# Kernel optimization log

Hardware: AMD Instinct MI355X
Metric: run time of the kernel (lower is better)

Reference implementation:

```python
import jax, jax.numpy as jnp
import numpy as np

ROT = 256  # Hadamard block size (ConvLinear4bit._n)


def _hadamard(n):
    # Sylvester construction of the n x n Hadamard matrix (n power of 2)
    H = np.array([[1.0]], dtype=np.float32)
    while H.shape[0] < n:
        H = np.block([[H, H], [H, -H]])
    return jnp.asarray(H / np.sqrt(n), dtype=jnp.float32)


def setup_inputs() -> dict:
    key = jax.random.key(0)
    k1, k2, k3, k4 = jax.random.split(key, 4)
    N, D_in, D_out = 4096, 4096, 4096
    x = jax.random.normal(k1, (N, D_in), dtype=jnp.float32)
    # unpacked int4 weights in [-7, 7] (logical content of the packed uint8 buffer)
    weight_int = jax.random.randint(k2, (D_out, D_in), -7, 8, dtype=jnp.int32)
    # per-output-row weight scales (quarot: max|W_rot| / 7)
    w_scale = jax.random.uniform(k3, (D_out, 1), dtype=jnp.float32) * 0.01 + 1e-4
    bias = jax.random.normal(k4, (D_out,), dtype=jnp.float32) * 0.01
    return {"x": x, "weight_int": weight_int, "w_scale": w_scale, "bias": bias}


def reference(x, weight_int, w_scale, bias):
    N, D = x.shape
    H = _hadamard(ROT)
    # blockwise Hadamard rotation along the feature dim (D is a multiple of ROT)
    x_rot = (x.reshape(N, D // ROT, ROT) @ H).reshape(N, D)
    # per-row symmetric int4 quantization of activations
    scales_x = jnp.max(jnp.abs(x_rot), axis=-1, keepdims=True) / 7.0  # [N, 1]
    q_x = jnp.clip(jnp.round(x_rot / scales_x), -8, 7).astype(jnp.int32)
    acc = jnp.matmul(q_x, weight_int.T)
    # sym_dequant: row scale (activations) * col scale (weights), then bias
    out = acc.astype(jnp.float32) * scales_x * w_scale.T + bias
    return out
```

## Files before the change

### kernel.cpp

```cpp
#include <hip/hip_runtime.h>
#include <math.h>

typedef int v4i  __attribute__((ext_vector_type(4)));
typedef int v16i __attribute__((ext_vector_type(16)));

#define DIM 4096
#define BM 256
#define BK 128
#define ATILE (BM * BK)
#define BUFSZ (2 * ATILE)

__device__ __forceinline__ void async16(const void* g, void* l) {
    __builtin_amdgcn_global_load_lds((__attribute__((address_space(1))) void*)(g),
                                     (__attribute__((address_space(3))) void*)(l),
                                     16, 0, 0);
}

#define VMCNT(N) asm volatile("s_waitcnt vmcnt(" #N ")" ::: "memory")
#define BARRIER() asm volatile("s_barrier" ::: "memory")

__global__ __launch_bounds__(256) void prep(const float* __restrict__ x,
                                            const int* __restrict__ w,
                                            signed char* __restrict__ q,
                                            signed char* __restrict__ w8,
                                            float* __restrict__ scales) {
    if (blockIdx.x >= 4096) {
        int i = (blockIdx.x - 4096) * 256 + threadIdx.x;
        int4 v = ((const int4*)w)[i];
        char4 c;
        c.x = (signed char)v.x; c.y = (signed char)v.y;
        c.z = (signed char)v.z; c.w = (signed char)v.w;
        ((char4*)w8)[i] = c;
        return;
    }
    const int row  = blockIdx.x;
    const int lane = threadIdx.x & 63;
    const int wave = threadIdx.x >> 6;
    const float4* xr4 = (const float4*)(x + (size_t)row * DIM);

    float sgn[6];
    #pragma unroll
    for (int i = 0; i < 6; ++i) sgn[i] = (lane & (1 << i)) ? -1.0f : 1.0f;

    float f[4][4];
    #pragma unroll
    for (int b = 0; b < 4; ++b) {
        const int blk = wave + 4 * b;
        float4 v = xr4[blk * 64 + lane];
        float t0 = v.x + v.y, t1 = v.x - v.y;
        float t2 = v.z + v.w, t3 = v.z - v.w;
        f[b][0] = t0 + t2; f[b][1] = t1 + t3;
        f[b][2] = t0 - t2; f[b][3] = t1 - t3;
        #pragma unroll
        for (int st = 0; st < 6; ++st) {
            const int m = 1 << st;
            #pragma unroll
            for (int j = 0; j < 4; ++j) {
                float p = __shfl_xor(f[b][j], m, 64);
                f[b][j] = fmaf(sgn[st], f[b][j], p);
            }
        }
    }

    float m = 0.0f;
    #pragma unroll
    for (int b = 0; b < 4; ++b)
        #pragma unroll
        for (int j = 0; j < 4; ++j) m = fmaxf(m, fabsf(f[b][j]));
    #pragma unroll
    for (int d = 32; d; d >>= 1) m = fmaxf(m, __shfl_xor(m, d, 64));
    __shared__ float sm[4];
    if (lane == 0) sm[wave] = m;
    __syncthreads();
    m = fmaxf(fmaxf(sm[0], sm[1]), fmaxf(sm[2], sm[3]));

    const float s = (m * 0.0625f) / 7.0f;
    if (threadIdx.x == 0) scales[row] = s;
    const float rinv = 7.0f / m;

    char4* qr4 = (char4*)(q + (size_t)row * DIM);
    #pragma unroll
    for (int b = 0; b < 4; ++b) {
        const int blk = wave + 4 * b;
        char4 c;
        int qi;
        qi = (int)rintf(f[b][0] * rinv); c.x = (signed char)min(7, max(-8, qi));
        qi = (int)rintf(f[b][1] * rinv); c.y = (signed char)min(7, max(-8, qi));
        qi = (int)rintf(f[b][2] * rinv); c.z = (signed char)min(7, max(-8, qi));
        qi = (int)rintf(f[b][3] * rinv); c.w = (signed char)min(7, max(-8, qi));
        qr4[blk * 64 + lane] = c;
    }
}

__global__ __launch_bounds__(512, 2) void gemm_q8(const signed char* __restrict__ A,
                                                  const signed char* __restrict__ B,
                                                  const float* __restrict__ rowScale,
                                                  const float* __restrict__ wscale,
                                                  const float* __restrict__ bias,
                                                  float* __restrict__ out) {
    __shared__ __align__(16) signed char S[2 * BUFSZ];

    const int flat = blockIdx.y * gridDim.x + blockIdx.x;
    const int xcd  = flat & 7;
    const int idx  = flat >> 3;
    const int bm   = ((xcd >> 1) << 2) + (idx & 3);
    const int bn   = ((xcd & 1) << 3) + (idx >> 2);

    const int t = threadIdx.x;
    const int lane = t & 63;
    const int wave = t >> 6;
    const int wm = (wave >> 2) * 128;
    const int wn = (wave & 3) * 64;
    const int l31 = lane & 31, lh = lane >> 5;

    const signed char* ga[4];
    const signed char* gb[4];
    int ldsA[4], ldsB[4];
    #pragma unroll
    for (int h = 0; h < 4; ++h) {
        const int cidx = t + 512 * h;
        const int row  = cidx >> 3;
        const int g    = (cidx & 7) ^ (row & 7);
        ga[h] = A + (size_t)(bm * BM + row) * DIM + g * 16;
        gb[h] = B + (size_t)(bn * BM + row) * DIM + g * 16;
        ldsA[h] = cidx * 16;
        ldsB[h] = ATILE + cidx * 16;
    }

    int offA[4][4], offB[2][4];
    #pragma unroll
    for (int i = 0; i < 4; ++i)
        #pragma unroll
        for (int s = 0; s < 4; ++s) {
            const int r = wm + i * 32 + l31;
            offA[i][s] = r * BK + (((2 * s + lh) ^ (r & 7)) * 16);
        }
    #pragma unroll
    for (int j = 0; j < 2; ++j)
        #pragma unroll
        for (int s = 0; s < 4; ++s) {
            const int c = wn + j * 32 + l31;
            offB[j][s] = ATILE + c * BK + (((2 * s + lh) ^ (c & 7)) * 16);
        }

    v16i acc[4][2] = {};

#define STAGE(P) do {                                                          \
        _Pragma("unroll")                                                      \
        for (int h = 0; h < 4; ++h) {                                          \
            async16(ga[h], &S[(P) * BUFSZ + ldsA[h]]); ga[h] += BK;            \
            async16(gb[h], &S[(P) * BUFSZ + ldsB[h]]); gb[h] += BK;            \
        }                                                                      \
    } while (0)

#define COMPUTE(P) do {                                                        \
        __builtin_amdgcn_s_setprio(1);                                         \
        _Pragma("unroll")                                                      \
        for (int s = 0; s < 4; ++s) {                                          \
            const v4i a0 = *(const v4i*)&S[(P) * BUFSZ + offA[0][s]];          \
            const v4i a1 = *(const v4i*)&S[(P) * BUFSZ + offA[1][s]];          \
            const v4i a2 = *(const v4i*)&S[(P) * BUFSZ + offA[2][s]];          \
            const v4i a3 = *(const v4i*)&S[(P) * BUFSZ + offA[3][s]];          \
            const v4i b0 = *(const v4i*)&S[(P) * BUFSZ + offB[0][s]];          \
            const v4i b1 = *(const v4i*)&S[(P) * BUFSZ + offB[1][s]];          \
            acc[0][0] = __builtin_amdgcn_mfma_i32_32x32x32_i8(a0, b0, acc[0][0], 0, 0, 0); \
            acc[0][1] = __builtin_amdgcn_mfma_i32_32x32x32_i8(a0, b1, acc[0][1], 0, 0, 0); \
            acc[1][0] = __builtin_amdgcn_mfma_i32_32x32x32_i8(a1, b0, acc[1][0], 0, 0, 0); \
            acc[1][1] = __builtin_amdgcn_mfma_i32_32x32x32_i8(a1, b1, acc[1][1], 0, 0, 0); \
            acc[2][0] = __builtin_amdgcn_mfma_i32_32x32x32_i8(a2, b0, acc[2][0], 0, 0, 0); \
            acc[2][1] = __builtin_amdgcn_mfma_i32_32x32x32_i8(a2, b1, acc[2][1], 0, 0, 0); \
            acc[3][0] = __builtin_amdgcn_mfma_i32_32x32x32_i8(a3, b0, acc[3][0], 0, 0, 0); \
            acc[3][1] = __builtin_amdgcn_mfma_i32_32x32x32_i8(a3, b1, acc[3][1], 0, 0, 0); \
        }                                                                      \
        __builtin_amdgcn_s_setprio(0);                                         \
    } while (0)

    STAGE(0);
    #pragma unroll 1
    for (int it = 0; it < 15; ++it) {
        STAGE(1); VMCNT(8); BARRIER(); COMPUTE(0); BARRIER();
        STAGE(0); VMCNT(8); BARRIER(); COMPUTE(1); BARRIER();
    }
    STAGE(1); VMCNT(8); BARRIER(); COMPUTE(0); BARRIER();
    VMCNT(0); BARRIER(); COMPUTE(1);

#undef STAGE
#undef COMPUTE

    #pragma unroll
    for (int j = 0; j < 2; ++j) {
        const int col = bn * BM + wn + j * 32 + l31;
        const float ws = wscale[col];
        const float bs = bias[col];
        #pragma unroll
        for (int i = 0; i < 4; ++i) {
            const int rb = bm * BM + wm + i * 32 + 4 * lh;
            #pragma unroll
            for (int r = 0; r < 16; ++r) {
                const int row = rb + (r & 3) + 8 * (r >> 2);
                out[(size_t)row * DIM + col] =
                    ((float)acc[i][j][r] * rowScale[row]) * ws + bs;
            }
        }
    }
}

extern "C" void kernel_launch(void* const* d_in, const int* in_sizes, int n_in,
                              void* d_out, int out_size, void* d_ws, size_t ws_size,
                              hipStream_t stream) {
    const float* x      = (const float*)d_in[0];
    const int*   wint   = (const int*)d_in[1];
    const float* wscale = (const float*)d_in[2];
    const float* bias   = (const float*)d_in[3];
    float* out = (float*)d_out;

    signed char* q8 = (signed char*)d_ws;
    signed char* w8 = q8 + (size_t)DIM * DIM;
    float* sx = (float*)(w8 + (size_t)DIM * DIM);

    prep<<<4096 + 16384, 256, 0, stream>>>(x, wint, q8, w8, sx);
    gemm_q8<<<dim3(DIM / BM, DIM / BM), 512, 0, stream>>>(q8, w8, sx, wscale, bias, out);
}
```

Measured before the change: 266.3 us.

## Load B fragments directly to registers and triple-buffer A in LDS with BK=64

The GEMM no longer stages the weight tile through LDS. Each wave loads its B fragments straight from global memory into registers, rotating through three register sets. A tiles are kept in LDS in a fragment-native layout, using three rotating buffers of K=64 with one barrier per stage, replacing the previous double-buffered K=128 swizzled layout. The goal is to cut LDS traffic, LDS footprint and the number of barriers. The cost is extra VGPRs and uncoalesced global reads of B that depend on L2 hits, with no LDS sharing of B across the two waves that use the same columns.

New measurement: 284.1 us. +6.7%, slower.

```diff
diff --git a/kernel.cpp b/kernel.cpp
--- a/kernel.cpp
+++ b/kernel.cpp
@@ -6,9 +6,8 @@
 
 #define DIM 4096
 #define BM 256
-#define BK 128
-#define ATILE (BM * BK)
-#define BUFSZ (2 * ATILE)
+#define BK 64
+#define ABUF 16384
 
 __device__ __forceinline__ void async16(const void* g, void* l) {
     __builtin_amdgcn_global_load_lds((__attribute__((address_space(1))) void*)(g),
@@ -98,7 +97,7 @@
                                                   const float* __restrict__ wscale,
                                                   const float* __restrict__ bias,
                                                   float* __restrict__ out) {
-    __shared__ __align__(16) signed char S[2 * BUFSZ];
+    __shared__ __align__(16) signed char S[3 * ABUF];
 
     const int flat = blockIdx.y * gridDim.x + blockIdx.x;
     const int xcd  = flat & 7;
@@ -113,78 +112,109 @@
     const int wn = (wave & 3) * 64;
     const int l31 = lane & 31, lh = lane >> 5;
 
-    const signed char* ga[4];
-    const signed char* gb[4];
-    int ldsA[4], ldsB[4];
-    #pragma unroll
-    for (int h = 0; h < 4; ++h) {
+    const signed char* ga[2];
+    int ldsA[2];
+    #pragma unroll
+    for (int h = 0; h < 2; ++h) {
         const int cidx = t + 512 * h;
-        const int row  = cidx >> 3;
-        const int g    = (cidx & 7) ^ (row & 7);
-        ga[h] = A + (size_t)(bm * BM + row) * DIM + g * 16;
-        gb[h] = B + (size_t)(bn * BM + row) * DIM + g * 16;
+        const int b    = cidx >> 6;
+        const int g    = b >> 1;
+        const int sH   = b & 1;
+        const int l    = cidx & 63;
+        const int row  = g * 32 + (l & 31);
+        const int kb   = sH * 32 + (l >> 5) * 16;
+        ga[h] = A + (size_t)(bm * BM + row) * DIM + kb;
         ldsA[h] = cidx * 16;
-        ldsB[h] = ATILE + cidx * 16;
-    }
-
-    int offA[4][4], offB[2][4];
-    #pragma unroll
-    for (int i = 0; i < 4; ++i)
-        #pragma unroll
-        for (int s = 0; s < 4; ++s) {
-            const int r = wm + i * 32 + l31;
-            offA[i][s] = r * BK + (((2 * s + lh) ^ (r & 7)) * 16);
-        }
+    }
+
+    const signed char* pb[4];
     #pragma unroll
     for (int j = 0; j < 2; ++j)
         #pragma unroll
-        for (int s = 0; s < 4; ++s) {
-            const int c = wn + j * 32 + l31;
-            offB[j][s] = ATILE + c * BK + (((2 * s + lh) ^ (c & 7)) * 16);
-        }
+        for (int s = 0; s < 2; ++s)
+            pb[j * 2 + s] = B + (size_t)(bn * BM + wn + j * 32 + l31) * DIM
+                              + s * 32 + lh * 16;
+
+    const signed char* rbA = &S[(wave >> 2) * 8192 + lane * 16];
 
     v16i acc[4][2] = {};
-
-#define STAGE(P) do {                                                          \
-        _Pragma("unroll")                                                      \
-        for (int h = 0; h < 4; ++h) {                                          \
-            async16(ga[h], &S[(P) * BUFSZ + ldsA[h]]); ga[h] += BK;            \
-            async16(gb[h], &S[(P) * BUFSZ + ldsB[h]]); gb[h] += BK;            \
+    v4i b0[4], b1[4], b2[4];
+
+#define STAGE_A(P3) do {                                                       \
+        async16(ga[0], &S[(P3) * ABUF + ldsA[0]]); ga[0] += BK;                \
+        async16(ga[1], &S[(P3) * ABUF + ldsA[1]]); ga[1] += BK;                \
+    } while (0)
+
+#define B_LOAD(BS) do {                                                        \
+        BS[0] = *(const v4i*)pb[0]; pb[0] += BK;                               \
+        BS[1] = *(const v4i*)pb[1]; pb[1] += BK;                               \
+        BS[2] = *(const v4i*)pb[2]; pb[2] += BK;                               \
+        BS[3] = *(const v4i*)pb[3]; pb[3] += BK;                               \
+    } while (0)
+
+#define COMPUTE(P3, BS) do {                                                   \
+        const signed char* rb = rbA + (P3) * ABUF;                             \
+        __builtin_amdgcn_s_setprio(1);                                         \
+        {                                                                      \
+            const v4i a0 = *(const v4i*)(rb);                                  \
+            const v4i a1 = *(const v4i*)(rb + 2048);                           \
+            const v4i a2 = *(const v4i*)(rb + 4096);                           \
+            const v4i a3 = *(const v4i*)(rb + 6144);                           \
+            acc[0][0] = __builtin_amdgcn_mfma_i32_32x32x32_i8(a0, BS[0], acc[0][0], 0, 0, 0); \
+            acc[0][1] = __builtin_amdgcn_mfma_i32_32x32x32_i8(a0, BS[2], acc[0][1], 0, 0, 0); \
+            acc[1][0] = __builtin_amdgcn_mfma_i32_32x32x32_i8(a1, BS[0], acc[1][0], 0, 0, 0); \
+            acc[1][1] = __builtin_amdgcn_mfma_i32_32x32x32_i8(a1, BS[2], acc[1][1], 0, 0, 0); \
+            acc[2][0] = __builtin_amdgcn_mfma_i32_32x32x32_i8(a2, BS[0], acc[2][0], 0, 0, 0); \
+            acc[2][1] = __builtin_amdgcn_mfma_i32_32x32x32_i8(a2, BS[2], acc[2][1], 0, 0, 0); \
+            acc[3][0] = __builtin_amdgcn_mfma_i32_32x32x32_i8(a3, BS[0], acc[3][0], 0, 0, 0); \
+            acc[3][1] = __builtin_amdgcn_mfma_i32_32x32x32_i8(a3, BS[2], acc[3][1], 0, 0, 0); \
         }                                                                      \
-    } while (0)
-
-#define COMPUTE(P) do {                                                        \
-        __builtin_amdgcn_s_setprio(1);                                         \
-        _Pragma("unroll")                                                      \
-        for (int s = 0; s < 4; ++s) {                                          \
-            const v4i a0 = *(const v4i*)&S[(P) * BUFSZ + offA[0][s]];          \
-            const v4i a1 = *(const v4i*)&S[(P) * BUFSZ + offA[1][s]];          \
-            const v4i a2 = *(const v4i*)&S[(P) * BUFSZ + offA[2][s]];          \
-            const v4i a3 = *(const v4i*)&S[(P) * BUFSZ + offA[3][s]];          \
-            const v4i b0 = *(const v4i*)&S[(P) * BUFSZ + offB[0][s]];          \
-            const v4i b1 = *(const v4i*)&S[(P) * BUFSZ + offB[1][s]];          \
-            acc[0][0] = __builtin_amdgcn_mfma_i32_32x32x32_i8(a0, b0, acc[0][0], 0, 0, 0); \
-            acc[0][1] = __builtin_amdgcn_mfma_i32_32x32x32_i8(a0, b1, acc[0][1], 0, 0, 0); \
-            acc[1][0] = __builtin_amdgcn_mfma_i32_32x32x32_i8(a1, b0, acc[1][0], 0, 0, 0); \
-            acc[1][1] = __builtin_amdgcn_mfma_i32_32x32x32_i8(a1, b1, acc[1][1], 0, 0, 0); \
-            acc[2][0] = __builtin_amdgcn_mfma_i32_32x32x32_i8(a2, b0, acc[2][0], 0, 0, 0); \
-            acc[2][1] = __builtin_amdgcn_mfma_i32_32x32x32_i8(a2, b1, acc[2][1], 0, 0, 0); \
-            acc[3][0] = __builtin_amdgcn_mfma_i32_32x32x32_i8(a3, b0, acc[3][0], 0, 0, 0); \
-            acc[3][1] = __builtin_amdgcn_mfma_i32_32x32x32_i8(a3, b1, acc[3][1], 0, 0, 0); \
+        {                                                                      \
+            const v4i a0 = *(const v4i*)(rb + 1024);                           \
+            const v4i a1 = *(const v4i*)(rb + 3072);                           \
+            const v4i a2 = *(const v4i*)(rb + 5120);                           \
+            const v4i a3 = *(const v4i*)(rb + 7168);                           \
+            acc[0][0] = __builtin_amdgcn_mfma_i32_32x32x32_i8(a0, BS[1], acc[0][0], 0, 0, 0); \
+            acc[0][1] = __builtin_amdgcn_mfma_i32_32x32x32_i8(a0, BS[3], acc[0][1], 0, 0, 0); \
+            acc[1][0] = __builtin_amdgcn_mfma_i32_32x32x32_i8(a1, BS[1], acc[1][0], 0, 0, 0); \
+            acc[1][1] = __builtin_amdgcn_mfma_i32_32x32x32_i8(a1, BS[3], acc[1][1], 0, 0, 0); \
+            acc[2][0] = __builtin_amdgcn_mfma_i32_32x32x32_i8(a2, BS[1], acc[2][0], 0, 0, 0); \
+            acc[2][1] = __builtin_amdgcn_mfma_i32_32x32x32_i8(a2, BS[3], acc[2][1], 0, 0, 0); \
+            acc[3][0] = __builtin_amdgcn_mfma_i32_32x32x32_i8(a3, BS[1], acc[3][0], 0, 0, 0); \
+            acc[3][1] = __builtin_amdgcn_mfma_i32_32x32x32_i8(a3, BS[3], acc[3][1], 0, 0, 0); \
         }                                                                      \
         __builtin_amdgcn_s_setprio(0);                                         \
     } while (0)
 
-    STAGE(0);
+#define SUB(P3, FILL3, BSU, BSF, VN) do {                                      \
+        VMCNT(VN); BARRIER();                                                  \
+        STAGE_A(FILL3);                                                        \
+        B_LOAD(BSF);                                                           \
+        COMPUTE(P3, BSU);                                                      \
+    } while (0)
+
+#define SUB_NS(P3, BSU, VN) do {                                               \
+        VMCNT(VN); BARRIER();                                                  \
+        COMPUTE(P3, BSU);                                                      \
+    } while (0)
+
+    STAGE_A(0); B_LOAD(b0);
+    STAGE_A(1); B_LOAD(b1);
     #pragma unroll 1
-    for (int it = 0; it < 15; ++it) {
-        STAGE(1); VMCNT(8); BARRIER(); COMPUTE(0); BARRIER();
-        STAGE(0); VMCNT(8); BARRIER(); COMPUTE(1); BARRIER();
-    }
-    STAGE(1); VMCNT(8); BARRIER(); COMPUTE(0); BARRIER();
-    VMCNT(0); BARRIER(); COMPUTE(1);
-
-#undef STAGE
+    for (int it = 0; it < 20; ++it) {
+        SUB(0, 2, b0, b2, 6);
+        SUB(1, 0, b1, b0, 6);
+        SUB(2, 1, b2, b1, 6);
+    }
+    SUB(0, 2, b0, b2, 6);
+    SUB(1, 0, b1, b0, 6);
+    SUB_NS(2, b2, 6);
+    SUB_NS(0, b0, 0);
+
+#undef SUB
+#undef SUB_NS
+#undef STAGE_A
+#undef B_LOAD
 #undef COMPUTE
 
     #pragma unroll
```
